# Optimization experiments

Measured on AMD Instinct MI355X. Metric: run time of the kernel, lower is better.

## Reference

```python
import jax, jax.numpy as jnp
import numpy as np

EPS = 1e-5  # instance-norm epsilon (NormalizeLayer over spatial axes)

def instance_norm(x):
    # normalize over spatial axes (1,2) per sample, per channel
    mean = jnp.mean(x, axis=(1, 2), keepdims=True)
    var = jnp.var(x, axis=(1, 2), keepdims=True)
    return (x - mean) / jnp.sqrt(var + EPS)

def l2norm(x, axis=-1):
    return x / jnp.sqrt(jnp.sum(x * x, axis=axis, keepdims=True) + 1e-12)

def setup_inputs() -> dict:
    key = jax.random.key(0)
    ks = jax.random.split(key, 5)
    B, H, W, C = 4, 64, 64, 256
    content = jax.random.normal(ks[0], (B, H, W, C), jnp.float32)
    style = jax.random.normal(ks[1], (B, H, W, C), jnp.float32)
    scale = 1.0 / np.sqrt(C)
    Wq = jax.random.normal(ks[2], (C, C), jnp.float32) * scale
    Wk = jax.random.normal(ks[3], (C, C), jnp.float32) * scale
    Wv = jax.random.normal(ks[4], (C, C), jnp.float32) * scale
    bq = jnp.zeros((C,), jnp.float32)
    bk = jnp.zeros((C,), jnp.float32)
    bv = jnp.zeros((C,), jnp.float32)
    return {"content": content, "style": style, "Wq": Wq, "bq": bq,
            "Wk": Wk, "bk": bk, "Wv": Wv, "bv": bv}

def reference(content, style, Wq, bq, Wk, bk, Wv, bv):
    B, H, W, C = content.shape
    N = H * W
    norm_content = instance_norm(content)
    norm_style = instance_norm(style)
    # 1x1 convs == per-pixel linear layers
    Q = (jnp.einsum('bhwc,cd->bhwd', norm_content, Wq) + bq).reshape(B, N, C)
    K = (jnp.einsum('bhwc,cd->bhwd', norm_style, Wk) + bk).reshape(B, N, C)
    V = (jnp.einsum('bhwc,cd->bhwd', style, Wv) + bv).reshape(B, N, C)
    # cosine-similarity attention (Dot with normalize=True)
    attn = jnp.einsum('bnc,bmc->bnm', l2norm(Q), l2norm(K))  # [B, N, N]
    A = jax.nn.softmax(attn, axis=-1)
    M = jnp.einsum('bnm,bmc->bnc', A, V)                 # weighted mean
    S2 = jnp.einsum('bnm,bmc->bnc', A, V * V) - M * M    # weighted variance
    S2 = jax.nn.relu(S2)
    # safe sqrt: grad-safe at exactly 0 (matches sqrt(relu(x)) values)
    S = jnp.where(S2 > 0, jnp.sqrt(jnp.where(S2 > 0, S2, 1.0)), 0.0)
    S = S.reshape(B, H, W, C)
    M = M.reshape(B, H, W, C)
    return S * norm_content + M
```

## Files before the change

kernel.cpp:

```cpp
#include <hip/hip_runtime.h>
#include <cstdint>

#define BB 4
#define NN 4096
#define CC 256

typedef __attribute__((ext_vector_type(8))) short bf16x8;
typedef __attribute__((ext_vector_type(4))) short bf16x4;
typedef __attribute__((ext_vector_type(4))) float f32x4;
typedef unsigned int u32;
typedef __attribute__((ext_vector_type(4))) u32 u32x4;

#define MFMA_FP8(a, b, c)  __builtin_amdgcn_mfma_f32_16x16x32_fp8_fp8((a), (b), (c), 0, 0, 0)

#define WAITCNT(vm, xp, lgkm) (((vm) & 0xF) | (((vm) >> 4) << 14) | ((xp) << 4) | ((lgkm) << 8))

__device__ __forceinline__ unsigned short f2bf(float f) {
  union { float f; unsigned u; } v; v.f = f;
  unsigned r = v.u + 0x7fffu + ((v.u >> 16) & 1u);
  return (unsigned short)(r >> 16);
}
__device__ __forceinline__ u32 pk4_fp8(float a, float b, float c, float d) {
  u32 v = (u32)__builtin_amdgcn_cvt_pk_fp8_f32(a, b, 0, false);
  v = (u32)__builtin_amdgcn_cvt_pk_fp8_f32(c, d, (int)v, true);
  return v;
}
__device__ __forceinline__ unsigned char fp8_1(float a) {
  return (unsigned char)(((u32)__builtin_amdgcn_cvt_pk_fp8_f32(a, a, 0, false)) & 0xff);
}

typedef __attribute__((address_space(3))) unsigned int lds_u32;
typedef __attribute__((address_space(1))) unsigned int glb_u32;

__device__ __forceinline__ void async_cp16(const void* g, void* l) {
  __builtin_amdgcn_global_load_lds((const glb_u32*)g,
                                   (lds_u32*)(unsigned)(unsigned long long)l,
                                   16, 0, 0);
}

__global__ __launch_bounds__(256) void transpose_w(const float* __restrict__ Wq,
                                                   const float* __restrict__ Wk,
                                                   const float* __restrict__ Wv,
                                                   unsigned char* __restrict__ Wt8) {
  __shared__ float sT[64 * 65];
  int blk = blockIdx.x;
  int z = blk / 16, tl = blk % 16;
  int c0 = (tl >> 2) * 64, d0 = (tl & 3) * 64;
  const float* W = (z == 0) ? Wq : ((z == 1) ? Wk : Wv);
  #pragma unroll
  for (int i = 0; i < 16; ++i) {
    int e = i * 256 + threadIdx.x;
    int c = e >> 6, d = e & 63;
    sT[c * 65 + d] = W[(size_t)(c0 + c) * CC + d0 + d];
  }
  __syncthreads();
  #pragma unroll
  for (int i = 0; i < 16; ++i) {
    int e = i * 256 + threadIdx.x;
    int d = e >> 6, c = e & 63;
    Wt8[(size_t)z * 65536 + (size_t)(d0 + d) * CC + c0 + c] = fp8_1(sT[c * 65 + d]);
  }
}

__global__ __launch_bounds__(256) void stats_partial(const float* __restrict__ content,
                                                     const float* __restrict__ style,
                                                     float* __restrict__ sums) {
  int blk = blockIdx.x;
  int t = blk >> 9, b = (blk >> 7) & 3, chunk = blk & 127;
  const float* X = t ? style : content;
  int c = threadIdx.x;
  const float* base = X + ((size_t)b * NN + (size_t)chunk * 32) * CC + c;
  float s = 0.f, ss = 0.f;
  #pragma unroll 8
  for (int r = 0; r < 32; ++r) {
    float x = base[(size_t)r * CC];
    s += x; ss += x * x;
  }
  atomicAdd(&sums[((t * 2 + 0) * BB + b) * CC + c], s);
  atomicAdd(&sums[((t * 2 + 1) * BB + b) * CC + c], ss);
}

__global__ __launch_bounds__(256) void stats_finalize(const float* __restrict__ sums,
                                                      float* __restrict__ stats) {
  int i = blockIdx.x * 256 + threadIdx.x;
  int t = i >> 10, bc = i & 1023;
  float s = sums[(t * 2 + 0) * 1024 + bc];
  float ss = sums[(t * 2 + 1) * 1024 + bc];
  float m = s * (1.0f / NN);
  float var = ss * (1.0f / NN) - m * m;
  stats[(t * 2 + 0) * 1024 + bc] = m;
  stats[(t * 2 + 1) * 1024 + bc] = rsqrtf(var + 1e-5f);
}

__global__ __launch_bounds__(256, 2) void qkv_kernel(
    const float* __restrict__ content, const float* __restrict__ style,
    const unsigned char* __restrict__ Wt8,
    const float* __restrict__ bq, const float* __restrict__ bk, const float* __restrict__ bv,
    const float* __restrict__ stats,
    unsigned char* __restrict__ Qn, unsigned char* __restrict__ Kn,
    unsigned char* __restrict__ Vct) {
  __shared__ __align__(16) char sW[32768];
  __shared__ __align__(16) char sX[32768];

  int tid = threadIdx.x;
  int wid = tid >> 6, lane = tid & 63, quad = lane >> 4, l16 = lane & 15;
  int uwid = __builtin_amdgcn_readfirstlane(wid);
  int tileid = blockIdx.x;
  int z = blockIdx.y;
  int gr0 = tileid * 128;
  int b = gr0 >> 12;

  const float* X = (z == 0) ? content : style;
  int statt = (z == 0) ? 0 : 1;
  const float* mean = stats + ((statt * 2 + 0) * BB + b) * CC;
  const float* rstd = stats + ((statt * 2 + 1) * BB + b) * CC;
  bool donorm = (z < 2);

  #pragma unroll
  for (int i = 0; i < 8; ++i) {
    int lin = i * 256 + tid;
    int row = lin >> 4, c16 = lin & 15;
    int c = c16 * 16;
    const float* xr = X + (size_t)(gr0 + row) * CC + c;
    f32x4 x0 = *(const f32x4*)(xr + 0);
    f32x4 x1 = *(const f32x4*)(xr + 4);
    f32x4 x2 = *(const f32x4*)(xr + 8);
    f32x4 x3 = *(const f32x4*)(xr + 12);
    if (donorm) {
      f32x4 m0 = *(const f32x4*)(mean + c + 0), r0 = *(const f32x4*)(rstd + c + 0);
      f32x4 m1 = *(const f32x4*)(mean + c + 4), r1 = *(const f32x4*)(rstd + c + 4);
      f32x4 m2 = *(const f32x4*)(mean + c + 8), r2 = *(const f32x4*)(rstd + c + 8);
      f32x4 m3 = *(const f32x4*)(mean + c + 12), r3 = *(const f32x4*)(rstd + c + 12);
      x0 = (x0 - m0) * r0; x1 = (x1 - m1) * r1;
      x2 = (x2 - m2) * r2; x3 = (x3 - m3) * r3;
    }
    u32x4 pk;
    pk.x = pk4_fp8(x0.x, x0.y, x0.z, x0.w);
    pk.y = pk4_fp8(x1.x, x1.y, x1.z, x1.w);
    pk.z = pk4_fp8(x2.x, x2.y, x2.z, x2.w);
    pk.w = pk4_fp8(x3.x, x3.y, x3.z, x3.w);
    *(u32x4*)(sX + row * 256 + ((c16 ^ (row & 15)) * 16)) = pk;
  }

  f32x4 zero4 = {0.f, 0.f, 0.f, 0.f};
  f32x4 acc[2][16];
  #pragma unroll
  for (int i = 0; i < 2; ++i)
    #pragma unroll
    for (int j = 0; j < 16; ++j) acc[i][j] = zero4;

  const unsigned char* wb = Wt8 + (size_t)z * 65536;

  for (int half = 0; half < 2; ++half) {
    __syncthreads();
    #pragma unroll
    for (int it = 0; it < 8; ++it) {
      int L = it * 256 + wid * 64 + lane;
      int d = L >> 3;
      int c16 = (L & 7) ^ (d & 7);
      async_cp16(wb + (size_t)d * 256 + half * 128 + c16 * 16,
                 sW + (size_t)(it * 256 + uwid * 64) * 16);
    }
    __syncthreads();

    long a[2][4];
    #pragma unroll
    for (int mf = 0; mf < 2; ++mf) {
      int row = wid * 32 + mf * 16 + l16;
      #pragma unroll
      for (int kc = 0; kc < 4; ++kc) {
        int chunk = half * 8 + kc * 2 + (quad >> 1);
        a[mf][kc] = *(const long*)(sX + row * 256 + ((chunk ^ (row & 15)) * 16) + (quad & 1) * 8);
      }
    }
    #pragma unroll
    for (int nf = 0; nf < 16; ++nf) {
      int d = nf * 16 + l16;
      #pragma unroll
      for (int kc = 0; kc < 4; ++kc) {
        long bw = *(const long*)(sW + d * 128 + (((kc * 2 + (quad >> 1)) ^ (d & 7)) * 16) + (quad & 1) * 8);
        acc[0][nf] = MFMA_FP8(a[0][kc], bw, acc[0][nf]);
        acc[1][nf] = MFMA_FP8(a[1][kc], bw, acc[1][nf]);
      }
    }
  }

  const float* bias = (z == 0) ? bq : ((z == 1) ? bk : bv);
  #pragma unroll
  for (int nf = 0; nf < 16; ++nf) {
    float bb_ = bias[nf * 16 + l16];
    #pragma unroll
    for (int mf = 0; mf < 2; ++mf) {
      acc[mf][nf].x += bb_; acc[mf][nf].y += bb_;
      acc[mf][nf].z += bb_; acc[mf][nf].w += bb_;
    }
  }

  if (z < 2) {
    unsigned char* O = (z == 0) ? Qn : Kn;
    #pragma unroll
    for (int mf = 0; mf < 2; ++mf) {
      f32x4 ss = zero4;
      #pragma unroll
      for (int nf = 0; nf < 16; ++nf) ss += acc[mf][nf] * acc[mf][nf];
      #pragma unroll
      for (int m = 1; m < 16; m <<= 1) {
        ss.x += __shfl_xor(ss.x, m, 64);
        ss.y += __shfl_xor(ss.y, m, 64);
        ss.z += __shfl_xor(ss.z, m, 64);
        ss.w += __shfl_xor(ss.w, m, 64);
      }
      f32x4 rq;
      rq.x = rsqrtf(ss.x + 1e-12f); rq.y = rsqrtf(ss.y + 1e-12f);
      rq.z = rsqrtf(ss.z + 1e-12f); rq.w = rsqrtf(ss.w + 1e-12f);
      int r0 = wid * 32 + mf * 16 + quad * 4;
      #pragma unroll
      for (int nf = 0; nf < 16; ++nf) {
        int col = nf * 16 + l16;
        u32 p01 = (u32)__builtin_amdgcn_cvt_pk_fp8_f32(acc[mf][nf].x * rq.x, acc[mf][nf].y * rq.y, 0, false);
        u32 p23 = (u32)__builtin_amdgcn_cvt_pk_fp8_f32(acc[mf][nf].z * rq.z, acc[mf][nf].w * rq.w, 0, false);
        O[(size_t)(gr0 + r0 + 0) * CC + col] = (unsigned char)(p01 & 0xff);
        O[(size_t)(gr0 + r0 + 1) * CC + col] = (unsigned char)((p01 >> 8) & 0xff);
        O[(size_t)(gr0 + r0 + 2) * CC + col] = (unsigned char)(p23 & 0xff);
        O[(size_t)(gr0 + r0 + 3) * CC + col] = (unsigned char)((p23 >> 8) & 0xff);
      }
    }
  } else {
    char* sOT = sX;
    int n_in_b = gr0 & (NN - 1);
    __syncthreads();
    #pragma unroll
    for (int pass = 0; pass < 2; ++pass) {
      #pragma unroll
      for (int mf = 0; mf < 2; ++mf) {
        int j = wid * 2 + mf;
        #pragma unroll
        for (int nf = 0; nf < 16; ++nf) {
          int col = nf * 16 + l16;
          f32x4 v = acc[mf][nf];
          f32x4 w = pass ? (v * v) : v;
          u32 pk = pk4_fp8(w.x, w.y, w.z, w.w);
          *(u32*)(sOT + col * 128 + ((j ^ (col & 7)) * 16) + quad * 4) = pk;
        }
      }
      __syncthreads();
      unsigned char* orow = Vct + ((size_t)(b * 512 + (pass ? 256 : 0) + tid)) * NN + n_in_b;
      #pragma unroll
      for (int j = 0; j < 8; ++j) {
        u32x4 val = *(const u32x4*)(sOT + tid * 128 + ((j ^ (tid & 7)) * 16));
        *(u32x4*)(orow + j * 16) = val;
      }
      __syncthreads();
    }
  }
}

__global__ __launch_bounds__(512, 4) void flash_kernel(
    const unsigned char* __restrict__ Qn,
    const unsigned char* __restrict__ Kn,
    const unsigned char* __restrict__ Vct,
    const float* __restrict__ content,
    const float* __restrict__ stats,
    float* __restrict__ out) {
  __shared__ __align__(16) char smem[32768 + 32768 + 4096 + 128];
  char* sKb = smem;
  char* sV  = smem + 32768;
  char* sPb = smem + 65536;
  float* sL = (float*)(smem + 69632);
  float* sE2 = (float*)smem;

  int tid = threadIdx.x;
  int wid = tid >> 6, lane = tid & 63, quad = lane >> 4, l16 = lane & 15;
  int uwid = __builtin_amdgcn_readfirstlane(wid);

  int id = blockIdx.x;
  int b = (id >> 1) & 3;
  int tile = ((id >> 3) << 1) | (id & 1);
  int q0 = tile * 32;

  int qh = (wid >> 2) * 16;
  int kb0 = (wid & 3) * 16;
  int cw = wid * 64;

  long qf[8];
  {
    int row = q0 + qh + l16;
    const unsigned char* base = Qn + (((size_t)b * NN + row) << 8);
    #pragma unroll
    for (int kf = 0; kf < 8; ++kf)
      qf[kf] = *(const long*)(base + kf * 32 + quad * 8);
  }
  __builtin_amdgcn_s_waitcnt(WAITCNT(0, 7, 15));

  if (tid < 32) sL[tid] = 0.f;

  const unsigned char* kbp = Kn + (((size_t)b * NN) << 8);
  const unsigned char* vbp = Vct + ((size_t)b * 512) * NN;

  auto stageK = [&](int k0, int buf) {
    char* dst = sKb + buf * 16384;
    #pragma unroll
    for (int it = 0; it < 2; ++it) {
      int L = it * 512 + wid * 64 + lane;
      int ky = L >> 4, s = L & 15;
      int c16 = s ^ (ky & 15);
      async_cp16(kbp + (((size_t)(k0 + ky)) << 8) + c16 * 16,
                 dst + (size_t)(it * 512 + uwid * 64) * 16);
    }
  };
  auto stageV = [&](int k0) {
    #pragma unroll
    for (int it = 0; it < 4; ++it) {
      int L = it * 512 + wid * 64 + lane;
      int r128 = L >> 3, s8 = L & 7;
      int x = s8 ^ (r128 & 7);
      int ch = (r128 << 1) | (x >> 2);
      int k16 = x & 3;
      async_cp16(vbp + (size_t)ch * NN + k0 + k16 * 16,
                 sV + (size_t)(it * 512 + uwid * 64) * 16);
    }
  };

  f32x4 zero4 = {0.f, 0.f, 0.f, 0.f};
  f32x4 om[2][4];
  #pragma unroll
  for (int i = 0; i < 2; ++i)
    #pragma unroll
    for (int j = 0; j < 4; ++j) om[i][j] = zero4;
  float Lr = 0.f;
  long vf[2][4];

  int krow = kb0 + l16;
  int krowoff = krow * 256;
  int khalf = (quad & 1) * 8;

  auto s_phase = [&](int kt) {
    const char* sKc = sKb + (kt & 1) * 16384;
    char* sPc = sPb + (kt & 1) * 2048;
    f32x4 ta = zero4, tb = zero4;
    #pragma unroll
    for (int kf = 0; kf < 8; kf += 2) {
      int sa = (kf * 2 + (quad >> 1)) ^ (krow & 15);
      long aka = *(const long*)(sKc + krowoff + sa * 16 + khalf);
      ta = MFMA_FP8(aka, qf[kf], ta);
      int sb = ((kf + 1) * 2 + (quad >> 1)) ^ (krow & 15);
      long akb = *(const long*)(sKc + krowoff + sb * 16 + khalf);
      tb = MFMA_FP8(akb, qf[kf + 1], tb);
    }
    f32x4 sv = ta + tb;
    float p0 = __expf(sv.x), p1 = __expf(sv.y), p2 = __expf(sv.z), p3 = __expf(sv.w);
    Lr += p0 + p1 + p2 + p3;
    u32 w = pk4_fp8(p0, p1, p2, p3);
    int q = qh + l16;
    int c = (kb0 >> 2) + quad;
    *(u32*)(sPc + q * 64 + ((c ^ (q & 14)) * 4)) = w;
    #pragma unroll
    for (int ks = 0; ks < 2; ++ks) {
      int c16 = ks * 2 + (quad >> 1);
      #pragma unroll
      for (int nf = 0; nf < 4; ++nf) {
        int ch = cw + nf * 16 + l16;
        vf[ks][nf] = *(const long*)(sV + (ch >> 1) * 128 +
                        (((ch & 1) * 4 + c16) ^ ((ch >> 1) & 7)) * 16 + khalf);
      }
    }
  };

  stageK(0, 0);  stageV(0);  stageK(64, 1);
  __builtin_amdgcn_s_waitcnt(WAITCNT(2, 7, 15));
  __builtin_amdgcn_s_barrier();
  s_phase(0);
  __builtin_amdgcn_s_waitcnt(WAITCNT(63, 7, 0));
  __builtin_amdgcn_s_barrier();

  for (int kt = 0; kt < 64; ++kt) {
    stageV(((kt + 1) & 63) * 64);
    stageK(((kt + 2) & 63) * 64, kt & 1);

    const char* sPc = sPb + (kt & 1) * 2048;
    long pf[2][2];
    #pragma unroll
    for (int ks = 0; ks < 2; ++ks)
      #pragma unroll
      for (int mf = 0; mf < 2; ++mf) {
        int q = mf * 16 + l16;
        int c = ks * 8 + quad * 2;
        pf[ks][mf] = *(const long*)(sPc + q * 64 + ((c ^ (q & 14)) * 4));
      }

    #pragma unroll
    for (int ks = 0; ks < 2; ++ks)
      #pragma unroll
      for (int nf = 0; nf < 4; ++nf)
        #pragma unroll
        for (int mf = 0; mf < 2; ++mf)
          om[mf][nf] = MFMA_FP8(pf[ks][mf], vf[ks][nf], om[mf][nf]);

    __builtin_amdgcn_s_waitcnt(WAITCNT(2, 7, 15));
    if (kt < 63) s_phase(kt + 1);

    __builtin_amdgcn_s_waitcnt(WAITCNT(63, 7, 0));
    __builtin_amdgcn_s_barrier();
  }

  Lr += __shfl_xor(Lr, 16, 64);
  Lr += __shfl_xor(Lr, 32, 64);
  if (quad == 0) atomicAdd(&sL[qh + l16], Lr);
  __builtin_amdgcn_s_waitcnt(WAITCNT(0, 7, 0));
  __builtin_amdgcn_s_barrier();

  if (wid >= 4) {
    #pragma unroll
    for (int mf = 0; mf < 2; ++mf) {
      #pragma unroll
      for (int nf = 0; nf < 4; ++nf) {
        int ch = (wid - 4) * 64 + nf * 16 + l16;
        int cidx = (mf * 4 + quad) ^ (ch & 7);
        *(f32x4*)(sE2 + ch * 32 + cidx * 4) = om[mf][nf];
      }
    }
  }
  __syncthreads();

  if (wid < 4) {
    const float* meanc = stats + (0 * BB + b) * CC;
    const float* rstdc = stats + (1 * BB + b) * CC;
    float linv[2][4];
    #pragma unroll
    for (int mf = 0; mf < 2; ++mf)
      #pragma unroll
      for (int r = 0; r < 4; ++r)
        linv[mf][r] = 1.0f / sL[mf * 16 + quad * 4 + r];
    #pragma unroll
    for (int nf = 0; nf < 4; ++nf) {
      int ch = cw + nf * 16 + l16;
      float mc = meanc[ch], rc = rstdc[ch];
      #pragma unroll
      for (int mf = 0; mf < 2; ++mf) {
        int cidx = (mf * 4 + quad) ^ (ch & 7);
        f32x4 vv = *(const f32x4*)(sE2 + ch * 32 + cidx * 4);
        f32x4 ov = om[mf][nf];
        #pragma unroll
        for (int r = 0; r < 4; ++r) {
          int row = mf * 16 + quad * 4 + r;
          float li = linv[mf][r];
          float ovr = (r == 0) ? ov.x : (r == 1) ? ov.y : (r == 2) ? ov.z : ov.w;
          float vvr = (r == 0) ? vv.x : (r == 1) ? vv.y : (r == 2) ? vv.z : vv.w;
          float M = ovr * li;
          float E2 = vvr * li;
          float S2 = E2 - M * M;
          float S = (S2 > 0.f) ? sqrtf(S2) : 0.f;
          size_t gi = (((size_t)b * NN + q0 + row) << 8) + ch;
          float xh = (content[gi] - mc) * rc;
          out[gi] = S * xh + M;
        }
      }
    }
  }
}

extern "C" void kernel_launch(void* const* d_in, const int* in_sizes, int n_in,
                              void* d_out, int out_size, void* d_ws, size_t ws_size,
                              hipStream_t stream) {
  const float* content = (const float*)d_in[0];
  const float* style   = (const float*)d_in[1];
  const float* Wq = (const float*)d_in[2];
  const float* bq = (const float*)d_in[3];
  const float* Wk = (const float*)d_in[4];
  const float* bk = (const float*)d_in[5];
  const float* Wv = (const float*)d_in[6];
  const float* bv = (const float*)d_in[7];
  char* ws = (char*)d_ws;

  float* sums        = (float*)(ws + 0);
  float* stats       = (float*)(ws + 16384);
  unsigned char* Wt8 = (unsigned char*)(ws + 32768);
  unsigned char* Qn  = (unsigned char*)(ws + 229376);
  unsigned char* Kn  = (unsigned char*)(ws + 4423680);
  unsigned char* Vct = (unsigned char*)(ws + 8617984);
  float* outp = (float*)d_out;

  hipMemsetAsync(d_ws, 0, 16384, stream);
  hipLaunchKernelGGL(transpose_w, dim3(48), dim3(256), 0, stream, Wq, Wk, Wv, Wt8);
  hipLaunchKernelGGL(stats_partial, dim3(1024), dim3(256), 0, stream, content, style, sums);
  hipLaunchKernelGGL(stats_finalize, dim3(8), dim3(256), 0, stream, sums, stats);
  hipLaunchKernelGGL(qkv_kernel, dim3(128, 3), dim3(256), 0, stream,
                     content, style, Wt8, bq, bk, bv, stats, Qn, Kn, Vct);
  hipLaunchKernelGGL(flash_kernel, dim3(512), dim3(512), 0, stream,
                     Qn, Kn, Vct, content, stats, outp);
}
```

Baseline: 225.6 us.

## Store V in MFMA fragment layout and load it directly from global memory

The producer kernel now writes the transposed V/V² fp8 tensor in a tiled layout that matches the MFMA B-operand fragment order per key tile. The flash kernel drops the async V staging into LDS and loads each V fragment straight from global memory into registers, which halves shared memory per block and removes the LDS round trip and its bank-conflict swizzle. In exchange, V reads now come from global or cache with a waitcnt placed before the PV MFMAs, so latency hiding depends on loads issued one iteration ahead. The producer's stores also become scattered 8-byte writes.

```diff
diff --git a/kernel.cpp b/kernel.cpp
--- a/kernel.cpp
+++ b/kernel.cpp
@@ -10,6 +10,7 @@
 typedef __attribute__((ext_vector_type(4))) float f32x4;
 typedef unsigned int u32;
 typedef __attribute__((ext_vector_type(4))) u32 u32x4;
+typedef __attribute__((ext_vector_type(2))) u32 u32x2;
 
 #define MFMA_FP8(a, b, c)  __builtin_amdgcn_mfma_f32_16x16x32_fp8_fp8((a), (b), (c), 0, 0, 0)
 
@@ -228,6 +229,7 @@
   } else {
     char* sOT = sX;
     int n_in_b = gr0 & (NN - 1);
+    int ktbase = n_in_b >> 6;
     __syncthreads();
     #pragma unroll
     for (int pass = 0; pass < 2; ++pass) {
@@ -244,11 +246,19 @@
         }
       }
       __syncthreads();
-      unsigned char* orow = Vct + ((size_t)(b * 512 + (pass ? 256 : 0) + tid)) * NN + n_in_b;
+      int ch = pass * 256 + tid;
+      unsigned char* vb = Vct + (size_t)b * 2097152 + (size_t)ch * 8;
       #pragma unroll
       for (int j = 0; j < 8; ++j) {
         u32x4 val = *(const u32x4*)(sOT + tid * 128 + ((j ^ (tid & 7)) * 16));
-        *(u32x4*)(orow + j * 16) = val;
+        int ktile = ktbase + (j >> 2);
+        int ks = (j >> 1) & 1;
+        int q0 = (j & 1) * 2;
+        unsigned char* basep = vb + (size_t)((ktile * 2 + ks) * 4 + q0) * 4096;
+        u32x2 lo; lo.x = val.x; lo.y = val.y;
+        u32x2 hi; hi.x = val.z; hi.y = val.w;
+        *(u32x2*)(basep) = lo;
+        *(u32x2*)(basep + 4096) = hi;
       }
       __syncthreads();
     }
@@ -262,11 +272,10 @@
     const float* __restrict__ content,
     const float* __restrict__ stats,
     float* __restrict__ out) {
-  __shared__ __align__(16) char smem[32768 + 32768 + 4096 + 128];
+  __shared__ __align__(16) char smem[32768 + 4096 + 128];
   char* sKb = smem;
-  char* sV  = smem + 32768;
-  char* sPb = smem + 65536;
-  float* sL = (float*)(smem + 69632);
+  char* sPb = smem + 32768;
+  float* sL = (float*)(smem + 36864);
   float* sE2 = (float*)smem;
 
   int tid = threadIdx.x;
@@ -295,7 +304,7 @@
   if (tid < 32) sL[tid] = 0.f;
 
   const unsigned char* kbp = Kn + (((size_t)b * NN) << 8);
-  const unsigned char* vbp = Vct + ((size_t)b * 512) * NN;
+  const unsigned char* vbp = Vct + (size_t)b * 2097152 + quad * 4096 + (size_t)(cw + l16) * 8;
 
   auto stageK = [&](int k0, int buf) {
     char* dst = sKb + buf * 16384;
@@ -306,18 +315,6 @@
       int c16 = s ^ (ky & 15);
       async_cp16(kbp + (((size_t)(k0 + ky)) << 8) + c16 * 16,
                  dst + (size_t)(it * 512 + uwid * 64) * 16);
-    }
-  };
-  auto stageV = [&](int k0) {
-    #pragma unroll
-    for (int it = 0; it < 4; ++it) {
-      int L = it * 512 + wid * 64 + lane;
-      int r128 = L >> 3, s8 = L & 7;
-      int x = s8 ^ (r128 & 7);
-      int ch = (r128 << 1) | (x >> 2);
-      int k16 = x & 3;
-      async_cp16(vbp + (size_t)ch * NN + k0 + k16 * 16,
-                 sV + (size_t)(it * 512 + uwid * 64) * 16);
     }
   };
 
@@ -354,19 +351,15 @@
     int q = qh + l16;
     int c = (kb0 >> 2) + quad;
     *(u32*)(sPc + q * 64 + ((c ^ (q & 14)) * 4)) = w;
-    #pragma unroll
-    for (int ks = 0; ks < 2; ++ks) {
-      int c16 = ks * 2 + (quad >> 1);
-      #pragma unroll
-      for (int nf = 0; nf < 4; ++nf) {
-        int ch = cw + nf * 16 + l16;
-        vf[ks][nf] = *(const long*)(sV + (ch >> 1) * 128 +
-                        (((ch & 1) * 4 + c16) ^ ((ch >> 1) & 7)) * 16 + khalf);
-      }
-    }
+    const unsigned char* vt = vbp + (size_t)kt * 32768;
+    #pragma unroll
+    for (int ks = 0; ks < 2; ++ks)
+      #pragma unroll
+      for (int nf = 0; nf < 4; ++nf)
+        vf[ks][nf] = *(const long*)(vt + ks * 16384 + nf * 128);
   };
 
-  stageK(0, 0);  stageV(0);  stageK(64, 1);
+  stageK(0, 0);  stageK(64, 1);
   __builtin_amdgcn_s_waitcnt(WAITCNT(2, 7, 15));
   __builtin_amdgcn_s_barrier();
   s_phase(0);
@@ -374,8 +367,9 @@
   __builtin_amdgcn_s_barrier();
 
   for (int kt = 0; kt < 64; ++kt) {
-    stageV(((kt + 1) & 63) * 64);
     stageK(((kt + 2) & 63) * 64, kt & 1);
+
+    __builtin_amdgcn_s_waitcnt(WAITCNT(2, 7, 15));
 
     const char* sPc = sPb + (kt & 1) * 2048;
     long pf[2][2];
@@ -396,7 +390,6 @@
         for (int mf = 0; mf < 2; ++mf)
           om[mf][nf] = MFMA_FP8(pf[ks][mf], vf[ks][nf], om[mf][nf]);
 
-    __builtin_amdgcn_s_waitcnt(WAITCNT(2, 7, 15));
     if (kt < 63) s_phase(kt + 1);
 
     __builtin_amdgcn_s_waitcnt(WAITCNT(63, 7, 0));
```

Result: faster. 206.7 us (-8.4%).
